# Optimization experiments

Measured on AMD Instinct MI355X. Metric: run time of the kernel, lower is better.

Reference implementation:

```python
import jax, jax.numpy as jnp
import numpy as np

B, S, E, F = 8, 2048, 1024, 4096
EPS = 1e-5


def _layer_norm(x, gamma, beta):
    mu = jnp.mean(x, axis=-1, keepdims=True)
    var = jnp.mean((x - mu) ** 2, axis=-1, keepdims=True)
    return (x - mu) * jax.lax.rsqrt(var + EPS) * gamma + beta


def setup_inputs() -> dict:
    key = jax.random.key(0)
    ks = jax.random.split(key, 16)
    s = 0.02
    return {
        "x": jax.random.normal(ks[0], (B, S, E), dtype=jnp.float32),
        "Wq": jax.random.normal(ks[1], (E, E), dtype=jnp.float32) * s,
        "bq": jnp.zeros((E,), dtype=jnp.float32),
        "Wk": jax.random.normal(ks[2], (E, E), dtype=jnp.float32) * s,
        "bk": jnp.zeros((E,), dtype=jnp.float32),
        "Wv": jax.random.normal(ks[3], (E, E), dtype=jnp.float32) * s,
        "bv": jnp.zeros((E,), dtype=jnp.float32),
        "gamma1": jnp.ones((E,), dtype=jnp.float32),
        "beta1": jnp.zeros((E,), dtype=jnp.float32),
        "W1": jax.random.normal(ks[4], (E, F), dtype=jnp.float32) * s,
        "b1": jnp.zeros((F,), dtype=jnp.float32),
        "W2": jax.random.normal(ks[5], (F, E), dtype=jnp.float32) * s,
        "b2": jnp.zeros((E,), dtype=jnp.float32),
        "gamma2": jnp.ones((E,), dtype=jnp.float32),
        "beta2": jnp.zeros((E,), dtype=jnp.float32),
    }


def reference(x, Wq, bq, Wk, bk, Wv, bv, gamma1, beta1, W1, b1, W2, b2, gamma2, beta2):
    # Single-head attention exactly as the torch forward (neurogenesis=False path).
    q = x @ Wq + bq  # [B,S,E]
    k = x @ Wk + bk
    v = x @ Wv + bv
    scores = jnp.einsum('bse,bte->bst', q, k) / jnp.sqrt(jnp.float32(E))
    attn = jax.nn.softmax(scores, axis=-1)
    attn_out = jnp.einsum('bst,bte->bse', attn, v)
    # dropout is identity in eval mode
    h = _layer_norm(x + attn_out, gamma1, beta1)
    ffn = jax.nn.relu(h @ W1 + b1) @ W2 + b2
    out = _layer_norm(h + ffn, gamma2, beta2)
    return (out, k, q, v)
```

## Files before the change

### kernel.cpp

```cpp
#include <hip/hip_runtime.h>
#include <hip/hip_bf16.h>
#include <stdint.h>

typedef __attribute__((ext_vector_type(8))) short s16x8;
typedef __attribute__((ext_vector_type(4))) float f32x4;

static constexpr int Bb = 8, Ss = 2048, Ee = 1024, Ff = 4096;
static constexpr int M_TOK = Bb * Ss;
static constexpr size_t OUT_SLOT = (size_t)M_TOK * Ee;

__device__ inline unsigned short f2bf(float f) {
  unsigned int u = __float_as_uint(f);
  unsigned int r = (u + 0x7FFFu + ((u >> 16) & 1u)) >> 16;
  return (unsigned short)r;
}
__device__ inline float bf2f(unsigned short h) {
  return __uint_as_float(((unsigned int)h) << 16);
}

__device__ inline void gload16(const unsigned short* g, const unsigned short* l) {
  __builtin_amdgcn_global_load_lds(
      (const __attribute__((address_space(1))) void*)g,
      (__attribute__((address_space(3))) void*)(unsigned short*)l, 16, 0, 0);
}

__global__ __launch_bounds__(256) void k_cvt_f32_bf16(const float* __restrict__ in,
                                                      unsigned short* __restrict__ out, int n4) {
  int i = blockIdx.x * blockDim.x + threadIdx.x;
  int stride = gridDim.x * blockDim.x;
  for (; i < n4; i += stride) {
    float4 v = ((const float4*)in)[i];
    ushort4 o;
    o.x = f2bf(v.x); o.y = f2bf(v.y); o.z = f2bf(v.z); o.w = f2bf(v.w);
    ((ushort4*)out)[i] = o;
  }
}

__global__ __launch_bounds__(256) void k_transpose_w(const float* __restrict__ in,
                                                     unsigned short* __restrict__ out,
                                                     int R, int C) {
  __shared__ float t[32][33];
  int c0 = blockIdx.x * 32, r0 = blockIdx.y * 32;
  int tx = threadIdx.x, ty = threadIdx.y;
  for (int i = ty; i < 32; i += 8)
    t[i][tx] = in[(size_t)(r0 + i) * C + c0 + tx];
  __syncthreads();
  for (int i = ty; i < 32; i += 8)
    out[(size_t)(c0 + i) * R + r0 + tx] = f2bf(t[tx][i]);
}

__global__ __launch_bounds__(256) void k_transpose_v(const unsigned short* __restrict__ v,
                                                     unsigned short* __restrict__ vT) {
  __shared__ unsigned short t[32][33];
  int b = blockIdx.z;
  const unsigned short* in = v + (size_t)b * Ss * Ee;
  unsigned short* out = vT + (size_t)b * Ee * Ss;
  int c0 = blockIdx.x * 32, r0 = blockIdx.y * 32;
  int tx = threadIdx.x, ty = threadIdx.y;
  for (int i = ty; i < 32; i += 8)
    t[i][tx] = in[(size_t)(r0 + i) * Ee + c0 + tx];
  __syncthreads();
  for (int i = ty; i < 32; i += 8)
    out[(size_t)(c0 + i) * Ss + r0 + tx] = t[tx][i];
}

template <bool WF32, bool WB16, bool RELU, bool HAS_BIAS>
__global__ __launch_bounds__(512, 2) void k_gemm256(const unsigned short* __restrict__ A,
                                                    const unsigned short* __restrict__ Bt,
                                                    float* __restrict__ Cf,
                                                    unsigned short* __restrict__ Cb,
                                                    const float* __restrict__ bias,
                                                    int M, int N, int K,
                                                    long aBatch, long bBatch, long cBatch,
                                                    float scale) {
  __shared__ unsigned short lds[4][2][256 * 32];
  const int tid = threadIdx.x;
  const int lane = tid & 63;
  const int wid = tid >> 6;
  const int wr = wid >> 2, wc = wid & 3;

  const int gx = gridDim.x, gy = gridDim.y;
  const int nwg = gx * gy;
  const int id = blockIdx.y * gx + blockIdx.x;
  const int qq = nwg >> 3;
  const int s = (id & 7) * qq + (id >> 3);
  const int g4 = s / (gy * 4);
  const int r4 = s - g4 * gy * 4;
  const int m0 = (g4 * 4 + (r4 & 3)) * 256;
  const int n0 = (r4 >> 2) * 256;
  const int z = blockIdx.z;
  A += (size_t)z * aBatch;
  Bt += (size_t)z * bBatch;

  const int srow = tid >> 2;
  const int csrc = (tid & 3) ^ (srow & 3);
  const unsigned short* ga0 = A + (size_t)(m0 + srow) * K + csrc * 8;
  const unsigned short* ga1 = A + (size_t)(m0 + 128 + srow) * K + csrc * 8;
  const unsigned short* gb0 = Bt + (size_t)(n0 + srow) * K + csrc * 8;
  const unsigned short* gb1 = Bt + (size_t)(n0 + 128 + srow) * K + csrc * 8;
  const int waveDst = (wid << 9);

  auto STAGE = [&](int step) {
    const int slot = step & 3;
    const size_t ko = (size_t)step << 5;
    const unsigned short* la = &lds[slot][0][0];
    const unsigned short* lb = &lds[slot][1][0];
    gload16(ga0 + ko, la + waveDst);
    gload16(ga1 + ko, la + 4096 + waveDst);
    gload16(gb0 + ko, lb + waveDst);
    gload16(gb1 + ko, lb + 4096 + waveDst);
  };

  f32x4 acc[8][4] = {};
  const int fr = lane & 15;
  const int cc = ((lane >> 4) ^ (fr & 3)) * 8;
  const int nt = K >> 5;

  auto RD_B = [&](int slot, s16x8* rb) {
    const unsigned short* lb = &lds[slot][1][0];
#pragma unroll
    for (int ni = 0; ni < 4; ++ni)
      rb[ni] = *(const s16x8*)(lb + ((wc * 64 + ni * 16 + fr) * 32 + cc));
  };
  auto PHASE_MM = [&](int slot, s16x8* rb) {
    const unsigned short* la = &lds[slot][0][0];
    __builtin_amdgcn_s_setprio(1);
    s16x8 ra[8];
#pragma unroll
    for (int mi = 0; mi < 8; ++mi)
      ra[mi] = *(const s16x8*)(la + ((wr * 128 + mi * 16 + fr) * 32 + cc));
#pragma unroll
    for (int mi = 0; mi < 8; ++mi)
#pragma unroll
      for (int ni = 0; ni < 4; ++ni)
        acc[mi][ni] = __builtin_amdgcn_mfma_f32_16x16x32_bf16(ra[mi], rb[ni], acc[mi][ni], 0, 0, 0);
    __builtin_amdgcn_s_setprio(0);
  };
  auto VMW = [&](int p) {
    const int rem = nt - p;
    if (rem > 3)      asm volatile("s_waitcnt vmcnt(8)" ::: "memory");
    else if (rem == 3) asm volatile("s_waitcnt vmcnt(4)" ::: "memory");
    else               asm volatile("s_waitcnt vmcnt(0)" ::: "memory");
  };

  s16x8 BA[4], BB[4];

  STAGE(0); STAGE(1); STAGE(2);
  asm volatile("s_waitcnt vmcnt(4)" ::: "memory");
  __builtin_amdgcn_s_barrier();
  asm volatile("" ::: "memory");
  RD_B(0, BA);

  for (int t = 0; t < nt; t += 2) {
    RD_B((t + 1) & 3, BB);
    if (t + 3 < nt) STAGE(t + 3);
    VMW(t);
    __builtin_amdgcn_s_barrier();
    asm volatile("" ::: "memory");
    PHASE_MM(t & 3, BA);
    asm volatile("" ::: "memory");
    __builtin_amdgcn_s_barrier();
    if (t + 2 < nt) RD_B((t + 2) & 3, BA);
    if (t + 4 < nt) STAGE(t + 4);
    VMW(t + 1);
    __builtin_amdgcn_s_barrier();
    asm volatile("" ::: "memory");
    PHASE_MM((t + 1) & 3, BB);
    asm volatile("" ::: "memory");
    __builtin_amdgcn_s_barrier();
  }

  const int er = lane & 15, eq = lane >> 4;
#pragma unroll
  for (int mi = 0; mi < 8; ++mi) {
#pragma unroll
    for (int ni = 0; ni < 4; ++ni) {
#pragma unroll
      for (int r = 0; r < 4; ++r) {
        int row = m0 + wr * 128 + mi * 16 + eq * 4 + r;
        int col = n0 + wc * 64 + ni * 16 + er;
        float v = acc[mi][ni][r] * scale;
        if (HAS_BIAS) v += bias[col];
        if (RELU) v = v > 0.f ? v : 0.f;
        size_t idx = (size_t)z * cBatch + (size_t)row * N + col;
        if (WF32) Cf[idx] = v;
        if (WB16) Cb[idx] = f2bf(v);
      }
    }
  }
}

__global__ __launch_bounds__(256) void k_softmax(unsigned short* __restrict__ sa) {
  __shared__ float red[4];
  const int row = blockIdx.x;
  const int tid = threadIdx.x;
  unsigned short* sr = sa + (size_t)row * Ss;
  ushort4 u0 = ((const ushort4*)sr)[tid];
  ushort4 u1 = ((const ushort4*)sr)[tid + 256];
  float e[8];
  e[0] = bf2f(u0.x); e[1] = bf2f(u0.y); e[2] = bf2f(u0.z); e[3] = bf2f(u0.w);
  e[4] = bf2f(u1.x); e[5] = bf2f(u1.y); e[6] = bf2f(u1.z); e[7] = bf2f(u1.w);
  float m = fmaxf(fmaxf(fmaxf(e[0], e[1]), fmaxf(e[2], e[3])),
                  fmaxf(fmaxf(e[4], e[5]), fmaxf(e[6], e[7])));
  for (int s = 1; s < 64; s <<= 1) m = fmaxf(m, __shfl_xor(m, s, 64));
  if ((tid & 63) == 0) red[tid >> 6] = m;
  __syncthreads();
  m = fmaxf(fmaxf(red[0], red[1]), fmaxf(red[2], red[3]));
  __syncthreads();
  float sum = 0.f;
#pragma unroll
  for (int j = 0; j < 8; ++j) { e[j] = __expf(e[j] - m); sum += e[j]; }
  for (int s = 1; s < 64; s <<= 1) sum += __shfl_xor(sum, s, 64);
  if ((tid & 63) == 0) red[tid >> 6] = sum;
  __syncthreads();
  sum = red[0] + red[1] + red[2] + red[3];
  float inv = 1.f / sum;
  ushort4 o0, o1;
  o0.x = f2bf(e[0] * inv); o0.y = f2bf(e[1] * inv);
  o0.z = f2bf(e[2] * inv); o0.w = f2bf(e[3] * inv);
  o1.x = f2bf(e[4] * inv); o1.y = f2bf(e[5] * inv);
  o1.z = f2bf(e[6] * inv); o1.w = f2bf(e[7] * inv);
  ((ushort4*)sr)[tid] = o0;
  ((ushort4*)sr)[tid + 256] = o1;
}

template <bool A_F32, bool OUT_F32>
__global__ __launch_bounds__(256) void k_ln(const void* __restrict__ a,
                                            const unsigned short* __restrict__ bb,
                                            const float* __restrict__ gamma,
                                            const float* __restrict__ beta,
                                            void* __restrict__ outp) {
  __shared__ float red[4];
  const int row = blockIdx.x;
  const int tid = threadIdx.x;
  float v[4];
  if (A_F32) {
    float4 av = ((const float4*)((const float*)a + (size_t)row * Ee))[tid];
    v[0] = av.x; v[1] = av.y; v[2] = av.z; v[3] = av.w;
  } else {
    ushort4 av = ((const ushort4*)((const unsigned short*)a + (size_t)row * Ee))[tid];
    v[0] = bf2f(av.x); v[1] = bf2f(av.y); v[2] = bf2f(av.z); v[3] = bf2f(av.w);
  }
  ushort4 bv = ((const ushort4*)(bb + (size_t)row * Ee))[tid];
  v[0] += bf2f(bv.x); v[1] += bf2f(bv.y); v[2] += bf2f(bv.z); v[3] += bf2f(bv.w);
  float s = v[0] + v[1] + v[2] + v[3];
  float q = v[0] * v[0] + v[1] * v[1] + v[2] * v[2] + v[3] * v[3];
  for (int sh = 1; sh < 64; sh <<= 1) {
    s += __shfl_xor(s, sh, 64);
    q += __shfl_xor(q, sh, 64);
  }
  if ((tid & 63) == 0) red[tid >> 6] = s;
  __syncthreads();
  s = red[0] + red[1] + red[2] + red[3];
  __syncthreads();
  if ((tid & 63) == 0) red[tid >> 6] = q;
  __syncthreads();
  q = red[0] + red[1] + red[2] + red[3];
  float mu = s * (1.f / Ee);
  float var = q * (1.f / Ee) - mu * mu;
  float rinv = rsqrtf(var + 1e-5f);
  int c = tid * 4;
  float o0 = (v[0] - mu) * rinv * gamma[c + 0] + beta[c + 0];
  float o1 = (v[1] - mu) * rinv * gamma[c + 1] + beta[c + 1];
  float o2 = (v[2] - mu) * rinv * gamma[c + 2] + beta[c + 2];
  float o3 = (v[3] - mu) * rinv * gamma[c + 3] + beta[c + 3];
  if (OUT_F32) {
    float4 o; o.x = o0; o.y = o1; o.z = o2; o.w = o3;
    ((float4*)((float*)outp + (size_t)row * Ee))[tid] = o;
  } else {
    ushort4 o;
    o.x = f2bf(o0); o.y = f2bf(o1); o.z = f2bf(o2); o.w = f2bf(o3);
    ((ushort4*)((unsigned short*)outp + (size_t)row * Ee))[tid] = o;
  }
}

extern "C" void kernel_launch(void* const* d_in, const int* in_sizes, int n_in,
                              void* d_out, int out_size, void* d_ws, size_t ws_size,
                              hipStream_t stream) {
  const float* x = (const float*)d_in[0];
  const float* Wq = (const float*)d_in[1];
  const float* bq = (const float*)d_in[2];
  const float* Wk = (const float*)d_in[3];
  const float* bk = (const float*)d_in[4];
  const float* Wv = (const float*)d_in[5];
  const float* bv = (const float*)d_in[6];
  const float* g1 = (const float*)d_in[7];
  const float* be1 = (const float*)d_in[8];
  const float* W1 = (const float*)d_in[9];
  const float* b1 = (const float*)d_in[10];
  const float* W2 = (const float*)d_in[11];
  const float* b2 = (const float*)d_in[12];
  const float* g2 = (const float*)d_in[13];
  const float* be2 = (const float*)d_in[14];

  float* out = (float*)d_out;
  float* kO = out + OUT_SLOT;
  float* qO = out + 2 * OUT_SLOT;
  float* vO = out + 3 * OUT_SLOT;

  char* ws = (char*)d_ws;
  unsigned short* xb  = (unsigned short*)(ws + 0);
  unsigned short* WqT = (unsigned short*)(ws + 33554432ull);
  unsigned short* WkT = (unsigned short*)(ws + 35651584ull);
  unsigned short* WvT = (unsigned short*)(ws + 37748736ull);
  unsigned short* W1T = (unsigned short*)(ws + 39845888ull);
  unsigned short* W2T = (unsigned short*)(ws + 48234496ull);
  unsigned short* qb  = (unsigned short*)(ws + 56623104ull);
  unsigned short* kb  = (unsigned short*)(ws + 90177536ull);
  unsigned short* vb  = (unsigned short*)(ws + 123731968ull);
  unsigned short* scb = (unsigned short*)(ws + 157286400ull);
  unsigned short* vT  = (unsigned short*)(ws + 224395264ull);
  unsigned short* ao  = (unsigned short*)(ws + 56623104ull);
  unsigned short* hb  = (unsigned short*)(ws + 90177536ull);
  unsigned short* f1b = (unsigned short*)(ws + 157286400ull);
  unsigned short* f2b = (unsigned short*)(ws + 123731968ull);

  dim3 tb(32, 8);
  k_cvt_f32_bf16<<<2048, 256, 0, stream>>>(x, xb, M_TOK * Ee / 4);
  k_transpose_w<<<dim3(32, 32), tb, 0, stream>>>(Wq, WqT, Ee, Ee);
  k_transpose_w<<<dim3(32, 32), tb, 0, stream>>>(Wk, WkT, Ee, Ee);
  k_transpose_w<<<dim3(32, 32), tb, 0, stream>>>(Wv, WvT, Ee, Ee);
  k_transpose_w<<<dim3(128, 32), tb, 0, stream>>>(W1, W1T, Ee, Ff);
  k_transpose_w<<<dim3(32, 128), tb, 0, stream>>>(W2, W2T, Ff, Ee);
  k_gemm256<true, true, false, true><<<dim3(64, 4, 1), 512, 0, stream>>>(
      xb, WqT, qO, qb, bq, M_TOK, Ee, Ee, 0, 0, 0, 1.f);
  k_gemm256<true, true, false, true><<<dim3(64, 4, 1), 512, 0, stream>>>(
      xb, WkT, kO, kb, bk, M_TOK, Ee, Ee, 0, 0, 0, 1.f);
  k_gemm256<true, true, false, true><<<dim3(64, 4, 1), 512, 0, stream>>>(
      xb, WvT, vO, vb, bv, M_TOK, Ee, Ee, 0, 0, 0, 1.f);
  k_gemm256<false, true, false, false><<<dim3(8, 8, 8), 512, 0, stream>>>(
      qb, kb, nullptr, scb, nullptr, Ss, Ss, Ee, (long)Ss * Ee, (long)Ss * Ee, (long)Ss * Ss,
      0.03125f);
  k_softmax<<<Bb * Ss, 256, 0, stream>>>(scb);
  k_transpose_v<<<dim3(32, 64, 8), tb, 0, stream>>>(vb, vT);
  k_gemm256<false, true, false, false><<<dim3(8, 4, 8), 512, 0, stream>>>(
      scb, vT, nullptr, ao, nullptr, Ss, Ee, Ss, (long)Ss * Ss, (long)Ee * Ss, (long)Ss * Ee, 1.f);
  k_ln<true, false><<<M_TOK, 256, 0, stream>>>(x, ao, g1, be1, hb);
  k_gemm256<false, true, true, true><<<dim3(64, 16, 1), 512, 0, stream>>>(
      hb, W1T, nullptr, f1b, b1, M_TOK, Ff, Ee, 0, 0, 0, 1.f);
  k_gemm256<false, true, false, true><<<dim3(64, 4, 1), 512, 0, stream>>>(
      f1b, W2T, nullptr, f2b, b2, M_TOK, Ee, Ff, 0, 0, 0, 1.f);
  k_ln<false, true><<<M_TOK, 256, 0, stream>>>(hb, f2b, g2, be2, out);
}
```

Before: 735.5 us.

## Fuse QKV projections into one GEMM and restructure the K-loop pipeline

The three Q/K/V projection GEMMs become a single N=3072 GEMM over concatenated transposed weights and a concatenated bias. A QKV epilogue routes each column block to the correct fp32 output slot and bf16 workspace buffer. The GEMM main loop is rewritten to process one K-step per iteration in two half-M MFMA phases, with A and B tile loads issued separately to interleave global-to-LDS traffic with compute. The LDS swizzle pattern is also changed to cut bank conflicts. Together these aim to reduce launch count and tail effects and to improve load/compute overlap, at the cost of more barriers per K-step.

```diff
diff --git a/kernel.cpp b/kernel.cpp
--- a/kernel.cpp
+++ b/kernel.cpp
@@ -34,6 +34,15 @@
     o.x = f2bf(v.x); o.y = f2bf(v.y); o.z = f2bf(v.z); o.w = f2bf(v.w);
     ((ushort4*)out)[i] = o;
   }
+}
+
+__global__ __launch_bounds__(256) void k_concat3(const float* __restrict__ a,
+                                                 const float* __restrict__ b,
+                                                 const float* __restrict__ c,
+                                                 float* __restrict__ out) {
+  int i = blockIdx.x * 256 + threadIdx.x;
+  const float* src = (i < 1024) ? a : (i < 2048) ? b : c;
+  out[i] = src[i & 1023];
 }
 
 __global__ __launch_bounds__(256) void k_transpose_w(const float* __restrict__ in,
@@ -64,7 +73,7 @@
     out[(size_t)(c0 + i) * Ss + r0 + tx] = t[tx][i];
 }
 
-template <bool WF32, bool WB16, bool RELU, bool HAS_BIAS>
+template <bool QKV, bool WF32, bool WB16, bool RELU, bool HAS_BIAS>
 __global__ __launch_bounds__(512, 2) void k_gemm256(const unsigned short* __restrict__ A,
                                                     const unsigned short* __restrict__ Bt,
                                                     float* __restrict__ Cf,
@@ -93,79 +102,81 @@
   Bt += (size_t)z * bBatch;
 
   const int srow = tid >> 2;
-  const int csrc = (tid & 3) ^ (srow & 3);
+  const int csrc = (tid & 3) ^ ((tid >> 3) & 3);
   const unsigned short* ga0 = A + (size_t)(m0 + srow) * K + csrc * 8;
   const unsigned short* ga1 = A + (size_t)(m0 + 128 + srow) * K + csrc * 8;
   const unsigned short* gb0 = Bt + (size_t)(n0 + srow) * K + csrc * 8;
   const unsigned short* gb1 = Bt + (size_t)(n0 + 128 + srow) * K + csrc * 8;
   const int waveDst = (wid << 9);
 
-  auto STAGE = [&](int step) {
+  auto STAGE_A = [&](int step) {
     const int slot = step & 3;
     const size_t ko = (size_t)step << 5;
     const unsigned short* la = &lds[slot][0][0];
-    const unsigned short* lb = &lds[slot][1][0];
     gload16(ga0 + ko, la + waveDst);
     gload16(ga1 + ko, la + 4096 + waveDst);
+  };
+  auto STAGE_B = [&](int step) {
+    const int slot = step & 3;
+    const size_t ko = (size_t)step << 5;
+    const unsigned short* lb = &lds[slot][1][0];
     gload16(gb0 + ko, lb + waveDst);
     gload16(gb1 + ko, lb + 4096 + waveDst);
   };
 
   f32x4 acc[8][4] = {};
   const int fr = lane & 15;
-  const int cc = ((lane >> 4) ^ (fr & 3)) * 8;
+  const int cc = ((lane >> 4) ^ ((fr >> 1) & 3)) * 8;
   const int nt = K >> 5;
 
-  auto RD_B = [&](int slot, s16x8* rb) {
+  STAGE_A(0); STAGE_B(0); STAGE_A(1); STAGE_B(1); STAGE_A(2); STAGE_B(2);
+  asm volatile("s_waitcnt vmcnt(8)" ::: "memory");
+  __builtin_amdgcn_s_barrier();
+  asm volatile("" ::: "memory");
+
+  for (int t = 0; t < nt; ++t) {
+    const int slot = t & 3;
+    const unsigned short* la = &lds[slot][0][0];
     const unsigned short* lb = &lds[slot][1][0];
+    s16x8 ra[4], rb[4];
 #pragma unroll
     for (int ni = 0; ni < 4; ++ni)
       rb[ni] = *(const s16x8*)(lb + ((wc * 64 + ni * 16 + fr) * 32 + cc));
-  };
-  auto PHASE_MM = [&](int slot, s16x8* rb) {
-    const unsigned short* la = &lds[slot][0][0];
+#pragma unroll
+    for (int mi = 0; mi < 4; ++mi)
+      ra[mi] = *(const s16x8*)(la + ((wr * 128 + mi * 16 + fr) * 32 + cc));
+    if (t + 3 < nt) {
+      STAGE_A(t + 3);
+      asm volatile("s_waitcnt vmcnt(6)" ::: "memory");
+    } else if (t + 2 < nt) {
+      asm volatile("s_waitcnt vmcnt(4)" ::: "memory");
+    } else {
+      asm volatile("s_waitcnt vmcnt(0)" ::: "memory");
+    }
+    __builtin_amdgcn_s_barrier();
+    asm volatile("" ::: "memory");
     __builtin_amdgcn_s_setprio(1);
-    s16x8 ra[8];
-#pragma unroll
-    for (int mi = 0; mi < 8; ++mi)
-      ra[mi] = *(const s16x8*)(la + ((wr * 128 + mi * 16 + fr) * 32 + cc));
-#pragma unroll
-    for (int mi = 0; mi < 8; ++mi)
+#pragma unroll
+    for (int mi = 0; mi < 4; ++mi)
 #pragma unroll
       for (int ni = 0; ni < 4; ++ni)
         acc[mi][ni] = __builtin_amdgcn_mfma_f32_16x16x32_bf16(ra[mi], rb[ni], acc[mi][ni], 0, 0, 0);
     __builtin_amdgcn_s_setprio(0);
-  };
-  auto VMW = [&](int p) {
-    const int rem = nt - p;
-    if (rem > 3)      asm volatile("s_waitcnt vmcnt(8)" ::: "memory");
-    else if (rem == 3) asm volatile("s_waitcnt vmcnt(4)" ::: "memory");
-    else               asm volatile("s_waitcnt vmcnt(0)" ::: "memory");
-  };
-
-  s16x8 BA[4], BB[4];
-
-  STAGE(0); STAGE(1); STAGE(2);
-  asm volatile("s_waitcnt vmcnt(4)" ::: "memory");
-  __builtin_amdgcn_s_barrier();
-  asm volatile("" ::: "memory");
-  RD_B(0, BA);
-
-  for (int t = 0; t < nt; t += 2) {
-    RD_B((t + 1) & 3, BB);
-    if (t + 3 < nt) STAGE(t + 3);
-    VMW(t);
+    asm volatile("" ::: "memory");
+    __builtin_amdgcn_s_barrier();
+#pragma unroll
+    for (int mi = 0; mi < 4; ++mi)
+      ra[mi] = *(const s16x8*)(la + ((wr * 128 + (mi + 4) * 16 + fr) * 32 + cc));
+    if (t + 3 < nt) STAGE_B(t + 3);
     __builtin_amdgcn_s_barrier();
     asm volatile("" ::: "memory");
-    PHASE_MM(t & 3, BA);
-    asm volatile("" ::: "memory");
-    __builtin_amdgcn_s_barrier();
-    if (t + 2 < nt) RD_B((t + 2) & 3, BA);
-    if (t + 4 < nt) STAGE(t + 4);
-    VMW(t + 1);
-    __builtin_amdgcn_s_barrier();
-    asm volatile("" ::: "memory");
-    PHASE_MM((t + 1) & 3, BB);
+    __builtin_amdgcn_s_setprio(1);
+#pragma unroll
+    for (int mi = 0; mi < 4; ++mi)
+#pragma unroll
+      for (int ni = 0; ni < 4; ++ni)
+        acc[mi + 4][ni] = __builtin_amdgcn_mfma_f32_16x16x32_bf16(ra[mi], rb[ni], acc[mi + 4][ni], 0, 0, 0);
+    __builtin_amdgcn_s_setprio(0);
     asm volatile("" ::: "memory");
     __builtin_amdgcn_s_barrier();
   }
@@ -182,9 +193,18 @@
         float v = acc[mi][ni][r] * scale;
         if (HAS_BIAS) v += bias[col];
         if (RELU) v = v > 0.f ? v : 0.f;
-        size_t idx = (size_t)z * cBatch + (size_t)row * N + col;
-        if (WF32) Cf[idx] = v;
-        if (WB16) Cb[idx] = f2bf(v);
+        if (QKV) {
+          int which = col >> 10;
+          int c2 = col & 1023;
+          size_t ro = (size_t)row * 1024 + c2;
+          int fslot = (which == 0) ? 2 : (which == 1) ? 1 : 3;
+          Cf[(size_t)fslot * OUT_SLOT + ro] = v;
+          Cb[(size_t)which * OUT_SLOT + ro] = f2bf(v);
+        } else {
+          size_t idx = (size_t)z * cBatch + (size_t)row * N + col;
+          if (WF32) Cf[idx] = v;
+          if (WB16) Cb[idx] = f2bf(v);
+        }
       }
     }
   }
@@ -294,51 +314,44 @@
   const float* be2 = (const float*)d_in[14];
 
   float* out = (float*)d_out;
-  float* kO = out + OUT_SLOT;
-  float* qO = out + 2 * OUT_SLOT;
-  float* vO = out + 3 * OUT_SLOT;
 
   char* ws = (char*)d_ws;
-  unsigned short* xb  = (unsigned short*)(ws + 0);
-  unsigned short* WqT = (unsigned short*)(ws + 33554432ull);
-  unsigned short* WkT = (unsigned short*)(ws + 35651584ull);
-  unsigned short* WvT = (unsigned short*)(ws + 37748736ull);
-  unsigned short* W1T = (unsigned short*)(ws + 39845888ull);
-  unsigned short* W2T = (unsigned short*)(ws + 48234496ull);
-  unsigned short* qb  = (unsigned short*)(ws + 56623104ull);
-  unsigned short* kb  = (unsigned short*)(ws + 90177536ull);
-  unsigned short* vb  = (unsigned short*)(ws + 123731968ull);
-  unsigned short* scb = (unsigned short*)(ws + 157286400ull);
-  unsigned short* vT  = (unsigned short*)(ws + 224395264ull);
-  unsigned short* ao  = (unsigned short*)(ws + 56623104ull);
-  unsigned short* hb  = (unsigned short*)(ws + 90177536ull);
-  unsigned short* f1b = (unsigned short*)(ws + 157286400ull);
-  unsigned short* f2b = (unsigned short*)(ws + 123731968ull);
+  unsigned short* xb    = (unsigned short*)(ws + 0);
+  unsigned short* WqkvT = (unsigned short*)(ws + 33554432ull);
+  unsigned short* W1T   = (unsigned short*)(ws + 39845888ull);
+  unsigned short* W2T   = (unsigned short*)(ws + 48234496ull);
+  unsigned short* qb    = (unsigned short*)(ws + 56623104ull);
+  unsigned short* kb    = (unsigned short*)(ws + 90177536ull);
+  unsigned short* vb    = (unsigned short*)(ws + 123731968ull);
+  unsigned short* scb   = (unsigned short*)(ws + 157286400ull);
+  unsigned short* vT    = (unsigned short*)(ws + 224395264ull);
+  float*          bqkv  = (float*)(ws + 257949696ull);
+  unsigned short* ao    = (unsigned short*)(ws + 56623104ull);
+  unsigned short* hb    = (unsigned short*)(ws + 90177536ull);
+  unsigned short* f1b   = (unsigned short*)(ws + 157286400ull);
+  unsigned short* f2b   = (unsigned short*)(ws + 123731968ull);
 
   dim3 tb(32, 8);
   k_cvt_f32_bf16<<<2048, 256, 0, stream>>>(x, xb, M_TOK * Ee / 4);
-  k_transpose_w<<<dim3(32, 32), tb, 0, stream>>>(Wq, WqT, Ee, Ee);
-  k_transpose_w<<<dim3(32, 32), tb, 0, stream>>>(Wk, WkT, Ee, Ee);
-  k_transpose_w<<<dim3(32, 32), tb, 0, stream>>>(Wv, WvT, Ee, Ee);
+  k_transpose_w<<<dim3(32, 32), tb, 0, stream>>>(Wq, WqkvT, Ee, Ee);
+  k_transpose_w<<<dim3(32, 32), tb, 0, stream>>>(Wk, WqkvT + 1048576, Ee, Ee);
+  k_transpose_w<<<dim3(32, 32), tb, 0, stream>>>(Wv, WqkvT + 2097152, Ee, Ee);
   k_transpose_w<<<dim3(128, 32), tb, 0, stream>>>(W1, W1T, Ee, Ff);
   k_transpose_w<<<dim3(32, 128), tb, 0, stream>>>(W2, W2T, Ff, Ee);
-  k_gemm256<true, true, false, true><<<dim3(64, 4, 1), 512, 0, stream>>>(
-      xb, WqT, qO, qb, bq, M_TOK, Ee, Ee, 0, 0, 0, 1.f);
-  k_gemm256<true, true, false, true><<<dim3(64, 4, 1), 512, 0, stream>>>(
-      xb, WkT, kO, kb, bk, M_TOK, Ee, Ee, 0, 0, 0, 1.f);
-  k_gemm256<true, true, false, true><<<dim3(64, 4, 1), 512, 0, stream>>>(
-      xb, WvT, vO, vb, bv, M_TOK, Ee, Ee, 0, 0, 0, 1.f);
-  k_gemm256<false, true, false, false><<<dim3(8, 8, 8), 512, 0, stream>>>(
+  k_concat3<<<12, 256, 0, stream>>>(bq, bk, bv, bqkv);
+  k_gemm256<true, true, true, false, true><<<dim3(64, 12, 1), 512, 0, stream>>>(
+      xb, WqkvT, out, qb, bqkv, M_TOK, 3072, Ee, 0, 0, 0, 1.f);
+  k_gemm256<false, false, true, false, false><<<dim3(8, 8, 8), 512, 0, stream>>>(
       qb, kb, nullptr, scb, nullptr, Ss, Ss, Ee, (long)Ss * Ee, (long)Ss * Ee, (long)Ss * Ss,
       0.03125f);
   k_softmax<<<Bb * Ss, 256, 0, stream>>>(scb);
   k_transpose_v<<<dim3(32, 64, 8), tb, 0, stream>>>(vb, vT);
-  k_gemm256<false, true, false, false><<<dim3(8, 4, 8), 512, 0, stream>>>(
+  k_gemm256<false, false, true, false, false><<<dim3(8, 4, 8), 512, 0, stream>>>(
       scb, vT, nullptr, ao, nullptr, Ss, Ee, Ss, (long)Ss * Ss, (long)Ee * Ss, (long)Ss * Ee, 1.f);
   k_ln<true, false><<<M_TOK, 256, 0, stream>>>(x, ao, g1, be1, hb);
-  k_gemm256<false, true, true, true><<<dim3(64, 16, 1), 512, 0, stream>>>(
+  k_gemm256<false, false, true, true, true><<<dim3(64, 16, 1), 512, 0, stream>>>(
       hb, W1T, nullptr, f1b, b1, M_TOK, Ff, Ee, 0, 0, 0, 1.f);
-  k_gemm256<false, true, false, true><<<dim3(64, 4, 1), 512, 0, stream>>>(
+  k_gemm256<false, false, true, false, true><<<dim3(64, 4, 1), 512, 0, stream>>>(
       f1b, W2T, nullptr, f2b, b2, M_TOK, Ee, Ff, 0, 0, 0, 1.f);
   k_ln<false, true><<<M_TOK, 256, 0, stream>>>(hb, f2b, g2, be2, out);
 }
```

New measurement: 692.7 us. 1.06x faster.
